# Kernel optimization log

Measured on AMD Instinct MI355X. Metric: run time of the kernel, lower is better.

The kernel has to match this reference:

```python
import jax, jax.numpy as jnp
import numpy as np

E = 1024   # embedding_dim
H = 64     # head_size
B, T = 8, 2048

def setup_inputs() -> dict:
    key = jax.random.key(0)
    k1, k2, k3, k4 = jax.random.split(key, 4)
    s = 1.0 / np.sqrt(E)
    return {
        "x": jax.random.normal(k1, (B, T, E), dtype=jnp.float32),
        "Wq": jax.random.normal(k2, (E, H), dtype=jnp.float32) * s,
        "Wk": jax.random.normal(k3, (E, H), dtype=jnp.float32) * s,
        "Wv": jax.random.normal(k4, (E, H), dtype=jnp.float32) * s,
    }

def reference(x, Wq, Wk, Wv):
    # projections: [B,T,E] @ [E,H] -> [B,T,H]
    q = x @ Wq
    k = x @ Wk
    v = x @ Wv
    Tq = x.shape[1]
    # scaled scores [B,T,T], masked causal softmax, then @ V
    wei = jnp.einsum('bth,bsh->bts', q, k) * (H ** -0.5)
    causal = jnp.tril(jnp.ones((Tq, Tq), dtype=bool))
    wei = jnp.where(causal, wei, -jnp.inf)
    attn = jax.nn.softmax(wei, axis=-1)
    return attn @ v
```

## Files before the change

kernel.cpp:

```cpp
#include <hip/hip_runtime.h>

#define E  1024
#define H  64
#define BB 8
#define TT 2048

typedef __attribute__((ext_vector_type(8)))  short bf16x8;
typedef __attribute__((ext_vector_type(4)))  float f32x4;
typedef __attribute__((ext_vector_type(16))) float f32x16;
typedef __attribute__((ext_vector_type(8)))  short short8;
typedef __attribute__((ext_vector_type(4)))  short short4v;
typedef __attribute__((ext_vector_type(4)))  unsigned u32x4;

__device__ __forceinline__ short f2bf(float f) {
    union { float f; unsigned u; } v; v.f = f;
    unsigned r = v.u + 0x7FFFu + ((v.u >> 16) & 1u);
    return (short)(r >> 16);
}

__device__ __forceinline__ float fexp2(float x) {
    float r;
    asm("v_exp_f32 %0, %1" : "=v"(r) : "v"(x));
    return r;
}

__global__ __launch_bounds__(256)
void pack_w(const float* __restrict__ Wq, const float* __restrict__ Wk,
            const float* __restrict__ Wv, short* __restrict__ Wb)
{
    const int t  = blockIdx.x * 256 + threadIdx.x;
    const int l  = t & 63;
    const int f  = (t >> 6) % 12;
    const int kc = t / 768;
    const float* W = (f < 4) ? Wq : ((f < 8) ? Wk : Wv);
    const int e0 = kc * 32 + ((l >> 4) << 3);
    const int n  = ((f & 3) << 4) + (l & 15);
    short8 o;
    #pragma unroll
    for (int j = 0; j < 8; ++j) o[j] = f2bf(W[(e0 + j) * 64 + n]);
    *(short8*)&Wb[(size_t)t * 8] = o;
}

__global__ __launch_bounds__(256)
void proj_mfma(const float* __restrict__ x, const short* __restrict__ Wb,
               short* __restrict__ q, short* __restrict__ k, short* __restrict__ vt)
{
    __shared__ float part[2][12][64][4];
    const int t   = threadIdx.x;
    const int l   = t & 63;
    const int wid = t >> 6;
    const int wm  = wid & 1, kh = wid >> 1;
    const long row0 = (long)blockIdx.x * 32 + wm * 16;
    const int l15 = l & 15, g = l >> 4;

    f32x4 acc[12];
    #pragma unroll
    for (int f = 0; f < 12; ++f) acc[f] = (f32x4){0.f, 0.f, 0.f, 0.f};

    const float* xp = x + (row0 + l15) * E + kh * 512 + g * 8;
    const short* wp = Wb + (size_t)(kh * 16) * 12 * 512 + (size_t)l * 8;

    for (int kc = 0; kc < 16; ++kc) {
        float4 a0 = *(const float4*)(xp);
        float4 a1 = *(const float4*)(xp + 4);
        xp += 32;
        bf16x8 af;
        af[0] = f2bf(a0.x); af[1] = f2bf(a0.y); af[2] = f2bf(a0.z); af[3] = f2bf(a0.w);
        af[4] = f2bf(a1.x); af[5] = f2bf(a1.y); af[6] = f2bf(a1.z); af[7] = f2bf(a1.w);
        #pragma unroll
        for (int f = 0; f < 12; ++f) {
            bf16x8 bf = *(const bf16x8*)(wp + (size_t)f * 512);
            acc[f] = __builtin_amdgcn_mfma_f32_16x16x32_bf16(af, bf, acc[f], 0, 0, 0);
        }
        wp += 12 * 512;
    }

    if (kh == 1) {
        #pragma unroll
        for (int f = 0; f < 12; ++f)
            *(f32x4*)&part[wm][f][l][0] = acc[f];
    }
    __syncthreads();
    if (kh == 0) {
        #pragma unroll
        for (int f = 0; f < 12; ++f)
            acc[f] += *(const f32x4*)&part[wm][f][l][0];
        #pragma unroll
        for (int f = 0; f < 12; ++f) {
            const int m = f >> 2;
            const int h = ((f & 3) << 4) + l15;
            if (m == 2) {
                const long row = row0 + g * 4;
                const long bb = row >> 11;
                const int  t0 = (int)(row & 2047);
                short4v pkt;
                #pragma unroll
                for (int r = 0; r < 4; ++r) pkt[r] = f2bf(acc[f][r]);
                *(short4v*)&vt[(bb * 64 + h) * TT + t0] = pkt;
            } else {
                short* base = (m == 0) ? q : k;
                const float sc = (m == 0) ? (0.125f * 1.44269504f) : 1.0f;
                #pragma unroll
                for (int r = 0; r < 4; ++r) {
                    const long row = row0 + g * 4 + r;
                    base[row * 64 + h] = f2bf(acc[f][r] * sc);
                }
            }
        }
    }
}

__global__ __launch_bounds__(512)
void attn_v8(const short* __restrict__ qg,
             const short* __restrict__ kg,
             const short* __restrict__ vtg,
             float* __restrict__ out)
{
    __shared__ float Op[8][32][66];
    __shared__ float Ml[8][32][2];

    const int t   = threadIdx.x;
    const int L   = t & 63;
    const int w   = t >> 6;
    const int bid = blockIdx.x;
    const int b   = bid & 7;
    const int pr  = bid >> 3;
    const int l31 = L & 31, hi = L >> 5;

    const int stA = pr, stB = 63 - pr;
    const int nA = stA + 1;
    int WA = (8 * nA + 32) / 65;
    WA = WA < 1 ? 1 : (WA > 7 ? 7 : WA);
    const int WB = 8 - WA;

    const bool isB  = (w >= WA);
    const int  st   = isB ? stB : stA;
    const int  q0   = st * 32;
    const int  strd = isB ? WB : WA;
    const int  c0   = isB ? (w - WA) : w;

    bf16x8 qf[4];
    {
        const short* qp = qg + ((long)b * TT + q0 + l31) * 64 + hi * 8;
        qf[0] = *(const bf16x8*)(qp);
        qf[1] = *(const bf16x8*)(qp + 16);
        qf[2] = *(const bf16x8*)(qp + 32);
        qf[3] = *(const bf16x8*)(qp + 48);
    }

    f32x16 o0 = {}, o1 = {};
    float mrun = -1e30f, lrun = 0.f;

    const short* kbase = kg  + ((long)b * TT + l31) * 64 + hi * 8;
    const short* vbase = vtg + ((long)b * 64 + l31) * TT + hi * 8;

    for (int ci = c0; ci <= st; ci += strd) {
        const int kvs = ci * 32;
        const short* kp = kbase + (long)kvs * 64;
        bf16x8 kf0 = *(const bf16x8*)(kp);
        bf16x8 kf1 = *(const bf16x8*)(kp + 16);
        bf16x8 kf2 = *(const bf16x8*)(kp + 32);
        bf16x8 kf3 = *(const bf16x8*)(kp + 48);
        const short* vp = vbase + kvs;
        bf16x8 vf00 = *(const bf16x8*)(vp);
        bf16x8 vf01 = *(const bf16x8*)(vp + 16);
        bf16x8 vf10 = *(const bf16x8*)(vp + 32 * TT);
        bf16x8 vf11 = *(const bf16x8*)(vp + 32 * TT + 16);

        f32x16 s = {};
        __builtin_amdgcn_s_setprio(1);
        s = __builtin_amdgcn_mfma_f32_32x32x16_bf16(kf0, qf[0], s, 0, 0, 0);
        s = __builtin_amdgcn_mfma_f32_32x32x16_bf16(kf1, qf[1], s, 0, 0, 0);
        s = __builtin_amdgcn_mfma_f32_32x32x16_bf16(kf2, qf[2], s, 0, 0, 0);
        s = __builtin_amdgcn_mfma_f32_32x32x16_bf16(kf3, qf[3], s, 0, 0, 0);
        __builtin_amdgcn_s_setprio(0);

        if (kvs == q0) {
            #pragma unroll
            for (int r = 0; r < 16; ++r) {
                const int crow = (r & 3) + 8 * (r >> 2) + 4 * hi;
                if (crow > l31) s[r] = -1e30f;
            }
        }
        float m01 = fmaxf(s[0], s[1]),   m23 = fmaxf(s[2], s[3]);
        float m45 = fmaxf(s[4], s[5]),   m67 = fmaxf(s[6], s[7]);
        float m89 = fmaxf(s[8], s[9]),   mab = fmaxf(s[10], s[11]);
        float mcd = fmaxf(s[12], s[13]), mef = fmaxf(s[14], s[15]);
        float mloc = fmaxf(fmaxf(fmaxf(m01, m23), fmaxf(m45, m67)),
                           fmaxf(fmaxf(m89, mab), fmaxf(mcd, mef)));
        mloc = fmaxf(mloc, __shfl_xor(mloc, 32));
        if (__any(mloc > mrun + 8.f)) {
            const float mnew = fmaxf(mrun, mloc);
            const float a = fexp2(mrun - mnew);
            mrun = mnew;
            lrun *= a;
            #pragma unroll
            for (int r = 0; r < 16; ++r) { o0[r] *= a; o1[r] *= a; }
        }
        #pragma unroll
        for (int r = 0; r < 16; ++r) s[r] = fexp2(s[r] - mrun);
        {
            float s01 = (s[0] + s[1]) + (s[2] + s[3]);
            float s23 = (s[4] + s[5]) + (s[6] + s[7]);
            float s45 = (s[8] + s[9]) + (s[10] + s[11]);
            float s67 = (s[12] + s[13]) + (s[14] + s[15]);
            float lsum = (s01 + s23) + (s45 + s67);
            lsum += __shfl_xor(lsum, 32);
            lrun += lsum;
        }
        unsigned wv[8];
        #pragma unroll
        for (int i = 0; i < 8; ++i)
            asm("v_cvt_pk_bf16_f32 %0, %1, %2" : "=v"(wv[i]) : "v"(s[2 * i]), "v"(s[2 * i + 1]));
        unsigned p00 = wv[0], p02 = wv[2];
        unsigned p01 = wv[1], p03 = wv[3];
        unsigned p10 = wv[4], p12 = wv[6];
        unsigned p11 = wv[5], p13 = wv[7];
        asm("v_permlane32_swap_b32 %0, %1" : "+v"(p00), "+v"(p02));
        asm("v_permlane32_swap_b32 %0, %1" : "+v"(p01), "+v"(p03));
        asm("v_permlane32_swap_b32 %0, %1" : "+v"(p10), "+v"(p12));
        asm("v_permlane32_swap_b32 %0, %1" : "+v"(p11), "+v"(p13));
        u32x4 pb0u = {p00, p01, p02, p03};
        u32x4 pb1u = {p10, p11, p12, p13};
        bf16x8 pb0, pb1;
        __builtin_memcpy(&pb0, &pb0u, 16);
        __builtin_memcpy(&pb1, &pb1u, 16);
        __builtin_amdgcn_s_setprio(1);
        o0 = __builtin_amdgcn_mfma_f32_32x32x16_bf16(vf00, pb0, o0, 0, 0, 0);
        o0 = __builtin_amdgcn_mfma_f32_32x32x16_bf16(vf01, pb1, o0, 0, 0, 0);
        o1 = __builtin_amdgcn_mfma_f32_32x32x16_bf16(vf10, pb0, o1, 0, 0, 0);
        o1 = __builtin_amdgcn_mfma_f32_32x32x16_bf16(vf11, pb1, o1, 0, 0, 0);
        __builtin_amdgcn_s_setprio(0);
    }

    #pragma unroll
    for (int r = 0; r < 16; ++r) {
        const int h = (r & 3) + 8 * (r >> 2) + 4 * hi;
        Op[w][l31][h]      = o0[r];
        Op[w][l31][32 + h] = o1[r];
    }
    if (hi == 0) {
        Ml[w][l31][0] = mrun;
        Ml[w][l31][1] = lrun;
    }
    __syncthreads();

    {
        const bool tb   = (w >= 4);
        const int  base = tb ? WA : 0;
        const int  cnt  = tb ? WB : WA;
        const long oq0  = (long)(tb ? stB : stA) * 32;
        #pragma unroll
        for (int rr = 0; rr < 8; ++rr) {
            const int row = (w & 3) * 8 + rr;
            float M = -1e30f;
            for (int j = 0; j < cnt; ++j)
                M = fmaxf(M, Ml[base + j][row][0]);
            float Ls = 0.f, val = 0.f;
            for (int j = 0; j < cnt; ++j) {
                const float a = fexp2(Ml[base + j][row][0] - M);
                Ls  += a * Ml[base + j][row][1];
                val += a * Op[base + j][row][L];
            }
            out[((long)b * TT + oq0 + row) * 64 + L] = val / Ls;
        }
    }
}

extern "C" void kernel_launch(void* const* d_in, const int* in_sizes, int n_in,
                              void* d_out, int out_size, void* d_ws, size_t ws_size,
                              hipStream_t stream)
{
    const float* x  = (const float*)d_in[0];
    const float* Wq = (const float*)d_in[1];
    const float* Wk = (const float*)d_in[2];
    const float* Wv = (const float*)d_in[3];
    float* out = (float*)d_out;

    const size_t n = (size_t)BB * TT * H;
    short* q  = (short*)d_ws;
    short* k  = q + n;
    short* vt = k + n;
    short* Wb = vt + n;

    pack_w   <<<dim3(96),  256, 0, stream>>>(Wq, Wk, Wv, Wb);
    proj_mfma<<<dim3(512), 256, 0, stream>>>(x, Wb, q, k, vt);
    attn_v8  <<<dim3(256), 512, 0, stream>>>(q, k, vt, out);
}
```

Before: 61.06 us.

## Split projection K-dimension four ways, prefetch x loads, use packed bf16 convert

The projection kernel now gives each block 16 rows and splits the 1024-wide reduction across four waves of 256 each, reduced through shared memory. Blocks double from 512 to 1024 for more parallelism. The x loads are software-prefetched one step ahead and fully unrolled. The manual float-to-bf16 rounding is replaced with the hardware v_cvt_pk_bf16_f32 instruction. Costs are more shared-memory reduction traffic and more weight reads per output row, since each block now covers half as many rows.

```diff
diff --git a/kernel.cpp b/kernel.cpp
--- a/kernel.cpp
+++ b/kernel.cpp
@@ -21,6 +21,18 @@
 __device__ __forceinline__ float fexp2(float x) {
     float r;
     asm("v_exp_f32 %0, %1" : "=v"(r) : "v"(x));
+    return r;
+}
+
+__device__ __forceinline__ bf16x8 cvt8(float4 a0, float4 a1) {
+    unsigned w0, w1, w2, w3;
+    asm("v_cvt_pk_bf16_f32 %0, %1, %2" : "=v"(w0) : "v"(a0.x), "v"(a0.y));
+    asm("v_cvt_pk_bf16_f32 %0, %1, %2" : "=v"(w1) : "v"(a0.z), "v"(a0.w));
+    asm("v_cvt_pk_bf16_f32 %0, %1, %2" : "=v"(w2) : "v"(a1.x), "v"(a1.y));
+    asm("v_cvt_pk_bf16_f32 %0, %1, %2" : "=v"(w3) : "v"(a1.z), "v"(a1.w));
+    u32x4 u = {w0, w1, w2, w3};
+    bf16x8 r;
+    __builtin_memcpy(&r, &u, 16);
     return r;
 }
 
@@ -42,49 +54,68 @@
 }
 
 __global__ __launch_bounds__(256)
-void proj_mfma(const float* __restrict__ x, const short* __restrict__ Wb,
-               short* __restrict__ q, short* __restrict__ k, short* __restrict__ vt)
+void proj_v2(const float* __restrict__ x, const short* __restrict__ Wb,
+             short* __restrict__ q, short* __restrict__ k, short* __restrict__ vt)
 {
-    __shared__ float part[2][12][64][4];
+    __shared__ float part[3][12][64][4];
     const int t   = threadIdx.x;
     const int l   = t & 63;
-    const int wid = t >> 6;
-    const int wm  = wid & 1, kh = wid >> 1;
-    const long row0 = (long)blockIdx.x * 32 + wm * 16;
+    const int kh  = t >> 6;
+    const long row0 = (long)blockIdx.x * 16;
     const int l15 = l & 15, g = l >> 4;
 
     f32x4 acc[12];
     #pragma unroll
     for (int f = 0; f < 12; ++f) acc[f] = (f32x4){0.f, 0.f, 0.f, 0.f};
 
-    const float* xp = x + (row0 + l15) * E + kh * 512 + g * 8;
-    const short* wp = Wb + (size_t)(kh * 16) * 12 * 512 + (size_t)l * 8;
-
-    for (int kc = 0; kc < 16; ++kc) {
-        float4 a0 = *(const float4*)(xp);
-        float4 a1 = *(const float4*)(xp + 4);
-        xp += 32;
-        bf16x8 af;
-        af[0] = f2bf(a0.x); af[1] = f2bf(a0.y); af[2] = f2bf(a0.z); af[3] = f2bf(a0.w);
-        af[4] = f2bf(a1.x); af[5] = f2bf(a1.y); af[6] = f2bf(a1.z); af[7] = f2bf(a1.w);
+    const float* xp  = x + (row0 + l15) * E + kh * 256 + g * 8;
+    const short* wb0 = Wb + (size_t)(kh * 8) * 12 * 512 + (size_t)l * 8;
+
+    float4 a0 = *(const float4*)(xp);
+    float4 a1 = *(const float4*)(xp + 4);
+    float4 a2 = *(const float4*)(xp + 32);
+    float4 a3 = *(const float4*)(xp + 36);
+
+    #pragma unroll
+    for (int pp = 0; pp < 4; ++pp) {
+        float4 b0, b1, b2, b3;
+        if (pp < 3) {
+            const float* xn = xp + (pp + 1) * 64;
+            b0 = *(const float4*)(xn);
+            b1 = *(const float4*)(xn + 4);
+            b2 = *(const float4*)(xn + 32);
+            b3 = *(const float4*)(xn + 36);
+        }
+        bf16x8 af0 = cvt8(a0, a1);
+        bf16x8 af1 = cvt8(a2, a3);
+        const short* wp = wb0 + (size_t)(pp * 2) * 12 * 512;
         #pragma unroll
         for (int f = 0; f < 12; ++f) {
             bf16x8 bf = *(const bf16x8*)(wp + (size_t)f * 512);
-            acc[f] = __builtin_amdgcn_mfma_f32_16x16x32_bf16(af, bf, acc[f], 0, 0, 0);
+            acc[f] = __builtin_amdgcn_mfma_f32_16x16x32_bf16(af0, bf, acc[f], 0, 0, 0);
         }
         wp += 12 * 512;
-    }
-
-    if (kh == 1) {
+        #pragma unroll
+        for (int f = 0; f < 12; ++f) {
+            bf16x8 bf = *(const bf16x8*)(wp + (size_t)f * 512);
+            acc[f] = __builtin_amdgcn_mfma_f32_16x16x32_bf16(af1, bf, acc[f], 0, 0, 0);
+        }
+        a0 = b0; a1 = b1; a2 = b2; a3 = b3;
+    }
+
+    if (kh > 0) {
         #pragma unroll
         for (int f = 0; f < 12; ++f)
-            *(f32x4*)&part[wm][f][l][0] = acc[f];
+            *(f32x4*)&part[kh - 1][f][l][0] = acc[f];
     }
     __syncthreads();
     if (kh == 0) {
         #pragma unroll
-        for (int f = 0; f < 12; ++f)
-            acc[f] += *(const f32x4*)&part[wm][f][l][0];
+        for (int f = 0; f < 12; ++f) {
+            acc[f] += *(const f32x4*)&part[0][f][l][0];
+            acc[f] += *(const f32x4*)&part[1][f][l][0];
+            acc[f] += *(const f32x4*)&part[2][f][l][0];
+        }
         #pragma unroll
         for (int f = 0; f < 12; ++f) {
             const int m = f >> 2;
@@ -283,7 +314,7 @@
     short* vt = k + n;
     short* Wb = vt + n;
 
-    pack_w   <<<dim3(96),  256, 0, stream>>>(Wq, Wk, Wv, Wb);
-    proj_mfma<<<dim3(512), 256, 0, stream>>>(x, Wb, q, k, vt);
-    attn_v8  <<<dim3(256), 512, 0, stream>>>(q, k, vt, out);
-}
+    pack_w  <<<dim3(96),   256, 0, stream>>>(Wq, Wk, Wv, Wb);
+    proj_v2 <<<dim3(1024), 256, 0, stream>>>(x, Wb, q, k, vt);
+    attn_v8 <<<dim3(256),  512, 0, stream>>>(q, k, vt, out);
+}
```

Result: slower. 64.85 us (+6.2%).

## Stage x tile in swizzled LDS and split projection outputs across eight waves

Applied to the files above, without the earlier changes.

The projection kernel now loads each 32-row slab of x with coalesced float4 reads, converts it to bf16 using packed hardware convert instructions, and stores it into a swizzled 64KB LDS buffer. Eight waves then split the work by row group and output-fragment group, each keeping only three accumulators over the full K=1024. This removes the previous split-K reduction through shared memory and the per-element software bf16 rounding. In exchange it uses more LDS per block, which may lower occupancy, and it relies on the hardware conversion's rounding behaviour.

```diff
diff --git a/kernel.cpp b/kernel.cpp
--- a/kernel.cpp
+++ b/kernel.cpp
@@ -21,6 +21,18 @@
 __device__ __forceinline__ float fexp2(float x) {
     float r;
     asm("v_exp_f32 %0, %1" : "=v"(r) : "v"(x));
+    return r;
+}
+
+__device__ __forceinline__ bf16x8 cvt8(float4 a0, float4 a1) {
+    unsigned w0, w1, w2, w3;
+    asm("v_cvt_pk_bf16_f32 %0, %1, %2" : "=v"(w0) : "v"(a0.x), "v"(a0.y));
+    asm("v_cvt_pk_bf16_f32 %0, %1, %2" : "=v"(w1) : "v"(a0.z), "v"(a0.w));
+    asm("v_cvt_pk_bf16_f32 %0, %1, %2" : "=v"(w2) : "v"(a1.x), "v"(a1.y));
+    asm("v_cvt_pk_bf16_f32 %0, %1, %2" : "=v"(w3) : "v"(a1.z), "v"(a1.w));
+    u32x4 u = {w0, w1, w2, w3};
+    bf16x8 r;
+    __builtin_memcpy(&r, &u, 16);
     return r;
 }
 
@@ -41,71 +53,76 @@
     *(short8*)&Wb[(size_t)t * 8] = o;
 }
 
-__global__ __launch_bounds__(256)
-void proj_mfma(const float* __restrict__ x, const short* __restrict__ Wb,
-               short* __restrict__ q, short* __restrict__ k, short* __restrict__ vt)
+__global__ __launch_bounds__(512)
+void proj_v3(const float* __restrict__ x, const short* __restrict__ Wb,
+             short* __restrict__ q, short* __restrict__ k, short* __restrict__ vt)
 {
-    __shared__ float part[2][12][64][4];
-    const int t   = threadIdx.x;
+    __shared__ short xs[32 * 1024];
+    const int t = threadIdx.x;
+    const long row0 = (long)blockIdx.x * 32;
+
+    {
+        float4 va[16];
+        #pragma unroll
+        for (int i = 0; i < 8; ++i) {
+            const int idx = i * 512 + t;
+            const int row = idx >> 7, u = idx & 127;
+            const float* p = x + (row0 + row) * E + u * 8;
+            va[i * 2]     = *(const float4*)(p);
+            va[i * 2 + 1] = *(const float4*)(p + 4);
+        }
+        #pragma unroll
+        for (int i = 0; i < 8; ++i) {
+            const int idx = i * 512 + t;
+            const int row = idx >> 7, u = idx & 127;
+            *(bf16x8*)&xs[row * 1024 + ((u ^ (row & 7)) << 3)] = cvt8(va[i * 2], va[i * 2 + 1]);
+        }
+    }
+    __syncthreads();
+
     const int l   = t & 63;
-    const int wid = t >> 6;
-    const int wm  = wid & 1, kh = wid >> 1;
-    const long row0 = (long)blockIdx.x * 32 + wm * 16;
+    const int w8  = t >> 6;
+    const int rg  = w8 >> 2, fg = w8 & 3;
     const int l15 = l & 15, g = l >> 4;
-
-    f32x4 acc[12];
+    const int arow  = rg * 16 + l15;
+    const int abase = arow * 1024;
+    const int aswz  = arow & 7;
+
+    f32x4 acc[3] = {(f32x4){0,0,0,0}, (f32x4){0,0,0,0}, (f32x4){0,0,0,0}};
+    const short* wb = Wb + ((size_t)(fg * 3) * 64 + l) * 8;
+
+    #pragma unroll 4
+    for (int kc = 0; kc < 32; ++kc) {
+        bf16x8 af = *(const bf16x8*)&xs[abase + (((kc * 4 + g) ^ aswz) << 3)];
+        const short* wp = wb + (size_t)kc * 12 * 512;
+        bf16x8 b0 = *(const bf16x8*)(wp);
+        bf16x8 b1 = *(const bf16x8*)(wp + 512);
+        bf16x8 b2 = *(const bf16x8*)(wp + 1024);
+        acc[0] = __builtin_amdgcn_mfma_f32_16x16x32_bf16(af, b0, acc[0], 0, 0, 0);
+        acc[1] = __builtin_amdgcn_mfma_f32_16x16x32_bf16(af, b1, acc[1], 0, 0, 0);
+        acc[2] = __builtin_amdgcn_mfma_f32_16x16x32_bf16(af, b2, acc[2], 0, 0, 0);
+    }
+
+    const long rowb = row0 + rg * 16;
     #pragma unroll
-    for (int f = 0; f < 12; ++f) acc[f] = (f32x4){0.f, 0.f, 0.f, 0.f};
-
-    const float* xp = x + (row0 + l15) * E + kh * 512 + g * 8;
-    const short* wp = Wb + (size_t)(kh * 16) * 12 * 512 + (size_t)l * 8;
-
-    for (int kc = 0; kc < 16; ++kc) {
-        float4 a0 = *(const float4*)(xp);
-        float4 a1 = *(const float4*)(xp + 4);
-        xp += 32;
-        bf16x8 af;
-        af[0] = f2bf(a0.x); af[1] = f2bf(a0.y); af[2] = f2bf(a0.z); af[3] = f2bf(a0.w);
-        af[4] = f2bf(a1.x); af[5] = f2bf(a1.y); af[6] = f2bf(a1.z); af[7] = f2bf(a1.w);
-        #pragma unroll
-        for (int f = 0; f < 12; ++f) {
-            bf16x8 bf = *(const bf16x8*)(wp + (size_t)f * 512);
-            acc[f] = __builtin_amdgcn_mfma_f32_16x16x32_bf16(af, bf, acc[f], 0, 0, 0);
-        }
-        wp += 12 * 512;
-    }
-
-    if (kh == 1) {
-        #pragma unroll
-        for (int f = 0; f < 12; ++f)
-            *(f32x4*)&part[wm][f][l][0] = acc[f];
-    }
-    __syncthreads();
-    if (kh == 0) {
-        #pragma unroll
-        for (int f = 0; f < 12; ++f)
-            acc[f] += *(const f32x4*)&part[wm][f][l][0];
-        #pragma unroll
-        for (int f = 0; f < 12; ++f) {
-            const int m = f >> 2;
-            const int h = ((f & 3) << 4) + l15;
-            if (m == 2) {
-                const long row = row0 + g * 4;
-                const long bb = row >> 11;
-                const int  t0 = (int)(row & 2047);
-                short4v pkt;
-                #pragma unroll
-                for (int r = 0; r < 4; ++r) pkt[r] = f2bf(acc[f][r]);
-                *(short4v*)&vt[(bb * 64 + h) * TT + t0] = pkt;
-            } else {
-                short* base = (m == 0) ? q : k;
-                const float sc = (m == 0) ? (0.125f * 1.44269504f) : 1.0f;
-                #pragma unroll
-                for (int r = 0; r < 4; ++r) {
-                    const long row = row0 + g * 4 + r;
-                    base[row * 64 + h] = f2bf(acc[f][r] * sc);
-                }
-            }
+    for (int fi = 0; fi < 3; ++fi) {
+        const int f = fg * 3 + fi;
+        const int m = f >> 2;
+        const int h = ((f & 3) << 4) + l15;
+        if (m == 2) {
+            const long row = rowb + g * 4;
+            const long bb = row >> 11;
+            const int  t0 = (int)(row & 2047);
+            short4v pkt;
+            #pragma unroll
+            for (int r = 0; r < 4; ++r) pkt[r] = f2bf(acc[fi][r]);
+            *(short4v*)&vt[(bb * 64 + h) * TT + t0] = pkt;
+        } else {
+            short* base = (m == 0) ? q : k;
+            const float sc = (m == 0) ? (0.125f * 1.44269504f) : 1.0f;
+            #pragma unroll
+            for (int r = 0; r < 4; ++r)
+                base[(rowb + g * 4 + r) * 64 + h] = f2bf(acc[fi][r] * sc);
         }
     }
 }
@@ -283,7 +300,7 @@
     short* vt = k + n;
     short* Wb = vt + n;
 
-    pack_w   <<<dim3(96),  256, 0, stream>>>(Wq, Wk, Wv, Wb);
-    proj_mfma<<<dim3(512), 256, 0, stream>>>(x, Wb, q, k, vt);
-    attn_v8  <<<dim3(256), 512, 0, stream>>>(q, k, vt, out);
-}
+    pack_w  <<<dim3(96),  256, 0, stream>>>(Wq, Wk, Wv, Wb);
+    proj_v3 <<<dim3(512), 512, 0, stream>>>(x, Wb, q, k, vt);
+    attn_v8 <<<dim3(256), 512, 0, stream>>>(q, k, vt, out);
+}
```

Result: faster. 58.27 us (-4.6%).
